# Kernel tuning notes

Measured on AMD Instinct MI355X. Metric: run time of the kernel, lower is better.

Reference implementation:

```python
import jax, jax.numpy as jnp
import numpy as np

B, T, N = 1024, 256, 64  # batch, seq_len, n_labels


def setup_inputs() -> dict:
    key = jax.random.key(0)
    k1, k2, k3, k4, k5 = jax.random.split(key, 5)
    emit = jax.random.normal(k1, (B, T, N), dtype=jnp.float32)
    lens = jax.random.randint(k2, (B,), T // 2, T + 1)
    mask = jnp.arange(T)[None, :] < lens[:, None]  # [B, T] bool, monotone
    trans = 0.1 * jax.random.normal(k3, (N, N), dtype=jnp.float32)
    strans = 0.1 * jax.random.normal(k4, (N,), dtype=jnp.float32)
    etrans = 0.1 * jax.random.normal(k5, (N,), dtype=jnp.float32)
    return {"emit": emit, "trans": trans, "strans": strans,
            "etrans": etrans, "mask": mask}


def reference(emit, trans, strans, etrans, mask):
    """CRF partition function (Tagger.get_logZ), summed over the batch."""
    lse = jax.scipy.special.logsumexp
    # row-normalize transitions in log space (as in the torch module)
    strans_n = strans - lse(strans)
    etrans_n = etrans - lse(etrans)
    trans_n = trans - lse(trans, axis=-1, keepdims=True)  # [N, N]

    e = jnp.transpose(emit, (1, 0, 2))  # [T, B, N]
    m = mask.T                          # [T, B]

    alpha0 = strans_n + e[0]            # [B, N]

    def step(alpha, xs):
        emit_t, mask_t = xs             # [B, N], [B]
        # scores[b, k] = logsumexp_j(alpha[b, j] + trans[j, k] + emit_t[b, k])
        scores = lse(alpha[:, :, None] + trans_n[None, :, :]
                     + emit_t[:, None, :], axis=1)
        alpha = jnp.where(mask_t[:, None], scores, alpha)
        return alpha, None

    alpha, _ = jax.lax.scan(step, alpha0, (e[1:], m[1:]))
    logZ = jnp.sum(lse(alpha + etrans_n, axis=1))
    return logZ
```

## Files before the change

kernel.cpp:

```cpp
#include <hip/hip_runtime.h>


#define CRF_B 1024
#define CRF_T 256
#define CRF_N 64

__device__ __forceinline__ float rl0(float x) {
    return __int_as_float(__builtin_amdgcn_readfirstlane(__float_as_int(x)));
}
__device__ __forceinline__ float rlane(float x, int j) {
    return __int_as_float(__builtin_amdgcn_readlane(__float_as_int(x), j));
}

__device__ __forceinline__ float wave_lse(float v) {
    float m = v;
    #pragma unroll
    for (int off = 1; off < 64; off <<= 1) m = fmaxf(m, __shfl_xor(m, off));
    float s = __expf(v - m);
    #pragma unroll
    for (int off = 1; off < 64; off <<= 1) s += __shfl_xor(s, off);
    return m + __logf(s);
}

__launch_bounds__(256, 1)
__attribute__((amdgpu_waves_per_eu(1, 1)))
__global__ void crf_fwd_kernel(const float* __restrict__ emit,
                               const float* __restrict__ trans,
                               const float* __restrict__ strans,
                               const float* __restrict__ etrans,
                               const unsigned char* __restrict__ mask_u8,
                               float* __restrict__ out)
{
    const int tid  = threadIdx.x;
    const int lane = tid & 63;
    const int wid  = tid >> 6;
    const int b    = blockIdx.x * 4 + wid;

    float rowlse_v;
    {
        const float* rowp = trans + lane * CRF_N;
        float m = -1e30f;
        #pragma unroll 8
        for (int k = 0; k < CRF_N; ++k) m = fmaxf(m, rowp[k]);
        float s = 0.f;
        #pragma unroll 8
        for (int k = 0; k < CRF_N; ++k) s += __expf(rowp[k] - m);
        rowlse_v = m + __logf(s);
    }

    float Ecol[CRF_N];
    #pragma unroll
    for (int j = 0; j < CRF_N; ++j)
        Ecol[j] = trans[j * CRF_N + lane] - rlane(rowlse_v, j);
    float cmx = -1e30f;
    #pragma unroll
    for (int j = 0; j < CRF_N; ++j) cmx = fmaxf(cmx, Ecol[j]);
    #pragma unroll
    for (int j = 0; j < CRF_N; ++j) Ecol[j] = __expf(Ecol[j] - cmx);

    const float sn = wave_lse(strans[lane]);

    int len;
    {
        int c8 = 0;
        #pragma unroll
        for (int q = 0; q < 4; ++q)
            c8 += (mask_u8[(size_t)b * CRF_T + q * 64 + lane] != 0) ? 1 : 0;
        for (int off = 1; off < 64; off <<= 1) c8 += __shfl_xor(c8, off);
        if (c8 >= 128) {
            len = c8;
        } else {
            const int* mi = (const int*)mask_u8;
            int ci = 0;
            #pragma unroll
            for (int q = 0; q < 4; ++q)
                ci += (mi[(size_t)b * CRF_T + q * 64 + lane] != 0) ? 1 : 0;
            for (int off = 1; off < 64; off <<= 1) ci += __shfl_xor(ci, off);
            len = ci;
        }
    }

    const float* eb = emit + (size_t)b * CRF_T * CRF_N;

    float alpha0 = (strans[lane] - sn) + eb[lane];
    float c0 = rl0(alpha0);
    float u  = __expf(alpha0 - c0);
    float R  = 1.0f;
    float Lacc = c0;

#define CRF_STEP(EE)                                                    \
    {                                                                   \
        float s0 = 0.f, s1 = 0.f, s2 = 0.f, s3 = 0.f;                   \
        _Pragma("unroll")                                               \
        for (int j = 0; j < CRF_N; j += 4) {                            \
            s0 = fmaf(rlane(u, j + 0), Ecol[j + 0], s0);                \
            s1 = fmaf(rlane(u, j + 1), Ecol[j + 1], s1);                \
            s2 = fmaf(rlane(u, j + 2), Ecol[j + 2], s2);                \
            s3 = fmaf(rlane(u, j + 3), Ecol[j + 3], s3);                \
        }                                                               \
        float s = (s0 + s1) + (s2 + s3);                                \
        u = s * (R * (EE));                                             \
        float u0 = rl0(u);                                              \
        R = __builtin_amdgcn_rcpf(u0);                                  \
        Lacc += __logf(u0);                                             \
    }

    float eN[8], eeC[8];
    #pragma unroll
    for (int d = 0; d < 8; ++d) eN[d] = eb[(size_t)(1 + d) * CRF_N + lane];
    #pragma unroll
    for (int d = 0; d < 8; ++d) eeC[d] = __expf(eN[d] + cmx);

    int t0 = 1;
    while (t0 + 8 <= len) {
        #pragma unroll
        for (int d = 0; d < 8; ++d) {
            int ti = t0 + 8 + d;
            ti = (ti < len) ? ti : (len - 1);
            eN[d] = eb[(size_t)ti * CRF_N + lane];
        }
        CRF_STEP(eeC[0]); CRF_STEP(eeC[1]);
        CRF_STEP(eeC[2]); CRF_STEP(eeC[3]);
        CRF_STEP(eeC[4]); CRF_STEP(eeC[5]);
        CRF_STEP(eeC[6]); CRF_STEP(eeC[7]);
        #pragma unroll
        for (int d = 0; d < 8; ++d) eeC[d] = __expf(eN[d] + cmx);
        t0 += 8;
    }
    {
        const int nrem = len - t0;
        #pragma unroll
        for (int d = 0; d < 8; ++d) {
            if (d >= nrem) break;
            CRF_STEP(eeC[d]);
        }
    }
#undef CRF_STEP

    const float en = wave_lse(etrans[lane]);
    float v = Lacc + __logf(u * R) + (etrans[lane] - en);
    float m = v;
    #pragma unroll
    for (int off = 1; off < 64; off <<= 1) m = fmaxf(m, __shfl_xor(m, off));
    float sum = __expf(v - m);
    #pragma unroll
    for (int off = 1; off < 64; off <<= 1) sum += __shfl_xor(sum, off);

    if (lane == 0) {
        atomicAdd(out, m + __logf(sum));
    }
}

extern "C" void kernel_launch(void* const* d_in, const int* in_sizes, int n_in,
                              void* d_out, int out_size, void* d_ws, size_t ws_size,
                              hipStream_t stream) {
    const float* emit   = (const float*)d_in[0];
    const float* trans  = (const float*)d_in[1];
    const float* strans = (const float*)d_in[2];
    const float* etrans = (const float*)d_in[3];
    const unsigned char* mask = (const unsigned char*)d_in[4];
    float* out = (float*)d_out;

    hipMemsetAsync(out, 0, sizeof(float), stream);
    crf_fwd_kernel<<<dim3(CRF_B / 4), dim3(256), 0, stream>>>(
        emit, trans, strans, etrans, mask, out);
}
```

Before: 167.2 us.

## Replace per-step log with product accumulation and periodic frexp renormalization

Drops the per-step logf on the serial critical path. The normalizers are now multiplied into a running product, which is renormalized every 4 steps with frexp into a mantissa and an integer exponent count, and the log is taken once at the end. The readlane broadcasts are also batched into groups of 16 ahead of the FMAs, and the emission prefetch depth drops from 8 to 4. The product of up to 3 extra steps between renormalizations could overflow or underflow if per-step normalizers are extreme, and the shallower prefetch may expose more memory latency.

```diff
diff --git a/kernel.cpp b/kernel.cpp
--- a/kernel.cpp
+++ b/kernel.cpp
@@ -86,51 +86,62 @@
     float c0 = rl0(alpha0);
     float u  = __expf(alpha0 - c0);
     float R  = 1.0f;
-    float Lacc = c0;
+    float Pm = 1.0f;
+    int   Eacc = 0;
+    const float c0_keep = c0;
 
-#define CRF_STEP(EE)                                                    \
-    {                                                                   \
-        float s0 = 0.f, s1 = 0.f, s2 = 0.f, s3 = 0.f;                   \
-        _Pragma("unroll")                                               \
-        for (int j = 0; j < CRF_N; j += 4) {                            \
-            s0 = fmaf(rlane(u, j + 0), Ecol[j + 0], s0);                \
-            s1 = fmaf(rlane(u, j + 1), Ecol[j + 1], s1);                \
-            s2 = fmaf(rlane(u, j + 2), Ecol[j + 2], s2);                \
-            s3 = fmaf(rlane(u, j + 3), Ecol[j + 3], s3);                \
-        }                                                               \
-        float s = (s0 + s1) + (s2 + s3);                                \
-        u = s * (R * (EE));                                             \
-        float u0 = rl0(u);                                              \
-        R = __builtin_amdgcn_rcpf(u0);                                  \
-        Lacc += __logf(u0);                                             \
+#define CRF_STEP(EE)                                                     \
+    {                                                                    \
+        float s0 = 0.f, s1 = 0.f, s2 = 0.f, s3 = 0.f;                    \
+        _Pragma("unroll")                                                \
+        for (int g = 0; g < 4; ++g) {                                    \
+            float w[16];                                                 \
+            _Pragma("unroll")                                            \
+            for (int i = 0; i < 16; ++i) w[i] = rlane(u, 16 * g + i);    \
+            _Pragma("unroll")                                            \
+            for (int i = 0; i < 16; i += 4) {                            \
+                s0 = fmaf(w[i + 0], Ecol[16 * g + i + 0], s0);           \
+                s1 = fmaf(w[i + 1], Ecol[16 * g + i + 1], s1);           \
+                s2 = fmaf(w[i + 2], Ecol[16 * g + i + 2], s2);           \
+                s3 = fmaf(w[i + 3], Ecol[16 * g + i + 3], s3);           \
+            }                                                            \
+        }                                                                \
+        float s = (s0 + s1) + (s2 + s3);                                 \
+        u = s * (R * (EE));                                              \
+        float u0 = rl0(u);                                               \
+        R = __builtin_amdgcn_rcpf(u0);                                   \
+        Pm *= u0;                                                        \
     }
 
-    float eN[8], eeC[8];
+    float eN[4], eeC[4];
     #pragma unroll
-    for (int d = 0; d < 8; ++d) eN[d] = eb[(size_t)(1 + d) * CRF_N + lane];
+    for (int d = 0; d < 4; ++d) eN[d] = eb[(size_t)(1 + d) * CRF_N + lane];
     #pragma unroll
-    for (int d = 0; d < 8; ++d) eeC[d] = __expf(eN[d] + cmx);
+    for (int d = 0; d < 4; ++d) eeC[d] = __expf(eN[d] + cmx);
 
     int t0 = 1;
-    while (t0 + 8 <= len) {
+    while (t0 + 4 <= len) {
         #pragma unroll
-        for (int d = 0; d < 8; ++d) {
-            int ti = t0 + 8 + d;
+        for (int d = 0; d < 4; ++d) {
+            int ti = t0 + 4 + d;
             ti = (ti < len) ? ti : (len - 1);
             eN[d] = eb[(size_t)ti * CRF_N + lane];
         }
         CRF_STEP(eeC[0]); CRF_STEP(eeC[1]);
         CRF_STEP(eeC[2]); CRF_STEP(eeC[3]);
-        CRF_STEP(eeC[4]); CRF_STEP(eeC[5]);
-        CRF_STEP(eeC[6]); CRF_STEP(eeC[7]);
+        {
+            int ex;
+            Pm = frexpf(Pm, &ex);
+            Eacc += ex;
+        }
         #pragma unroll
-        for (int d = 0; d < 8; ++d) eeC[d] = __expf(eN[d] + cmx);
-        t0 += 8;
+        for (int d = 0; d < 4; ++d) eeC[d] = __expf(eN[d] + cmx);
+        t0 += 4;
     }
     {
         const int nrem = len - t0;
         #pragma unroll
-        for (int d = 0; d < 8; ++d) {
+        for (int d = 0; d < 4; ++d) {
             if (d >= nrem) break;
             CRF_STEP(eeC[d]);
         }
@@ -138,6 +149,7 @@
 #undef CRF_STEP
 
     const float en = wave_lse(etrans[lane]);
+    float Lacc = c0_keep + 0.6931471805599453f * (float)Eacc + __logf(Pm);
     float v = Lacc + __logf(u * R) + (etrans[lane] - en);
     float m = v;
     #pragma unroll
```

Result: faster. 158.0 us (-5.5%).
